# Optimization experiments

Hardware: AMD Instinct MI355X
Metric: run time of the kernel (lower is better)

## Reference

```python
import jax, jax.numpy as jnp
import numpy as np

B, NINP, NMAX, C = 32, 16, 128, 128

def conv1x1(x, w, b):
    # x: [B, cin, n, n], w: [cout, cin], b: [cout]
    return jnp.einsum('bchw,oc->bohw', x, w) + b[None, :, None, None]

def block(x, Msum, wa, ba, wb, bb, wc, bc):
    x1 = jax.nn.relu(conv1x1(x, wa, ba) * Msum)
    x2 = jax.nn.relu(conv1x1(x, wb, bb) * Msum)
    x1x2 = jnp.matmul(x1, x2) * Msum          # batched [B,C,n,n] @ [B,C,n,n]
    return jax.nn.relu(conv1x1(jnp.concatenate([x1x2, x], axis=1), wc, bc) * Msum)

def setup_inputs() -> dict:
    key = jax.random.key(0)
    ks = jax.random.split(key, 32)
    def w(k, o, i, s=0.05):
        return jax.random.normal(k, (o, i), dtype=jnp.float32) * s
    inp = {
        'X2': jax.random.normal(ks[0], (B, NINP, NMAX, NMAX), dtype=jnp.float32),
        'M':  jax.random.uniform(ks[1], (B, 2, NMAX, NMAX), dtype=jnp.float32),
        'w11': w(ks[2], C, NINP), 'b11': jnp.zeros((C,), jnp.float32),
        'w12': w(ks[3], C, NINP), 'b12': jnp.zeros((C,), jnp.float32),
        'w13': w(ks[4], C, C + NINP), 'b13': jnp.zeros((C,), jnp.float32),
        'w21': w(ks[5], C, C), 'b21': jnp.zeros((C,), jnp.float32),
        'w22': w(ks[6], C, C), 'b22': jnp.zeros((C,), jnp.float32),
        'w23': w(ks[7], C, 2 * C), 'b23': jnp.zeros((C,), jnp.float32),
        'w31': w(ks[8], C, C), 'b31': jnp.zeros((C,), jnp.float32),
        'w32': w(ks[9], C, C), 'b32': jnp.zeros((C,), jnp.float32),
        'w33': w(ks[10], C, 2 * C), 'b33': jnp.zeros((C,), jnp.float32),
        'h1w': w(ks[11], 32, 3 * C), 'h1b': jnp.zeros((32,), jnp.float32),
        'h2w': w(ks[12], 1, 32), 'h2b': jnp.zeros((1,), jnp.float32),
    }
    return inp

def reference(X2, M, w11, b11, w12, b12, w13, b13, w21, b21, w22, b22, w23, b23,
              w31, b31, w32, b32, w33, b33, h1w, h1b, h2w, h2b):
    Msum = jnp.sum(M, axis=1, keepdims=True)   # [B,1,n,n]
    Mdiag = M[:, 0:1]                          # [B,1,n,n]
    x = X2
    x = block(x, Msum, w11, b11, w12, b12, w13, b13)
    xo1 = jnp.sum(x * Mdiag, axis=(2, 3))      # [B,C]
    x = block(x, Msum, w21, b21, w22, b22, w23, b23)
    xo2 = jnp.sum(x * Mdiag, axis=(2, 3))
    x = block(x, Msum, w31, b31, w32, b32, w33, b33)
    xo3 = jnp.sum(x * Mdiag, axis=(2, 3))
    h = jnp.concatenate([xo1, xo2, xo3], axis=1)
    h = jax.nn.relu(h @ h1w.T + h1b)
    return h @ h2w.T + h2b                     # [B,1]
```

## Files before the change

### kernel.cpp

```cpp
#include <hip/hip_runtime.h>
#include <stdint.h>
#include <stddef.h>

#define NBATCH 32
#define HW     16384
#define CCH    128

typedef short bf16x8 __attribute__((ext_vector_type(8)));
typedef float f32x4  __attribute__((ext_vector_type(4)));

__device__ __forceinline__ float bf2f(unsigned short u){
    union { unsigned int i; float f; } v; v.i = ((unsigned int)u) << 16; return v.f;
}
__device__ __forceinline__ unsigned short f2bf(float f){
    union { float f; unsigned int i; } v; v.f = f;
    unsigned int x = v.i;
    x += 0x7fffu + ((x >> 16) & 1u);
    return (unsigned short)(x >> 16);
}

#define WPREP_TOTAL 319488
__global__ __launch_bounds__(256) void k_prep(
    const float* __restrict__ w11, const float* __restrict__ w12, const float* __restrict__ w13,
    const float* __restrict__ w21, const float* __restrict__ w22, const float* __restrict__ w23,
    const float* __restrict__ w31, const float* __restrict__ w32, const float* __restrict__ w33,
    unsigned short* __restrict__ wp)
{
    int i = blockIdx.x*256 + threadIdx.x;
    if(i >= WPREP_TOTAL) return;
    float v; int half;
    if(i < 16384){
        int j = i; half = (j >> 13) & 1;
        int r = (j >> 5) & 255, c = j & 31, col = c & 15;
        v = (r < 128) ? w11[r*16 + col] : w12[(r-128)*16 + col];
    } else if(i < 57344){
        int j = i - 16384; int ck = j >> 13; int jj = j & 8191;
        half = jj >> 12;
        int r = (jj >> 5) & 127, c = jj & 31;
        int col = (ck < 4) ? (ck*32 + c) : (128 + (c & 15));
        v = w13[r*144 + col];
    } else if(i < 122880){
        int j = i - 57344; int ck = j >> 14; int jj = j & 16383;
        half = jj >> 13;
        int r = (jj >> 5) & 255, c = jj & 31, col = ck*32 + c;
        v = (r < 128) ? w21[r*128 + col] : w22[(r-128)*128 + col];
    } else if(i < 188416){
        int j = i - 122880; int ck = j >> 13; int jj = j & 8191;
        half = jj >> 12;
        int r = (jj >> 5) & 127, c = jj & 31, col = ck*32 + c;
        v = w23[r*256 + col];
    } else if(i < 253952){
        int j = i - 188416; int ck = j >> 14; int jj = j & 16383;
        half = jj >> 13;
        int r = (jj >> 5) & 255, c = jj & 31, col = ck*32 + c;
        v = (r < 128) ? w31[r*128 + col] : w32[(r-128)*128 + col];
    } else {
        int j = i - 253952; int ck = j >> 13; int jj = j & 8191;
        half = jj >> 12;
        int r = (jj >> 5) & 127, c = jj & 31, col = ck*32 + c;
        v = w33[r*256 + col];
    }
    unsigned short hi = f2bf(v);
    wp[i] = half ? f2bf(v - bf2f(hi)) : hi;
}

__global__ __launch_bounds__(256) void k_xprep(const float* __restrict__ X2, unsigned short* __restrict__ X2b){
    int i = blockIdx.x*256 + threadIdx.x;
    int hw = i & (HW-1);
    int rest = i >> 14;
    int c = rest & 15, b = rest >> 4;
    float v = X2[i];
    unsigned short hi = f2bf(v);
    size_t dst = (size_t)b*32*HW + (size_t)c*HW + hw;
    X2b[dst] = hi;
    X2b[dst + (size_t)16*HW] = f2bf(v - bf2f(hi));
}

__global__ __launch_bounds__(256) void k_msum(const float* __restrict__ M, float* __restrict__ msum){
    int i = blockIdx.x*256 + threadIdx.x;
    int b = i >> 14, hw = i & (HW-1);
    msum[i] = M[(size_t)b*2*HW + hw] + M[(size_t)b*2*HW + HW + hw];
}

template<int NCH, int CIN, bool GX>
__global__ __launch_bounds__(256,2) void k_cab(
    const unsigned short* __restrict__ Wp,
    const unsigned short* __restrict__ xin,
    const float* __restrict__ ba, const float* __restrict__ bb,
    const float* __restrict__ msum,
    unsigned short* __restrict__ A, unsigned short* __restrict__ Bm, int b0)
{
    __shared__ unsigned short Wlh[256*40];
    __shared__ unsigned short Wll[256*40];
    __shared__ unsigned short Xt[128*40];
    const int bi = blockIdx.y, bg = b0 + bi;
    const int hw0 = blockIdx.x * 128;
    const int t = threadIdx.x;
    const int w = t >> 6, l = t & 63;
    const int lr = l & 15, lg = l >> 4;
    const unsigned short* xbase = xin + (size_t)(GX ? bg : bi)*CIN*HW;

    f32x4 acc[4][8];
    #pragma unroll
    for(int mf=0; mf<4; mf++)
        #pragma unroll
        for(int nf=0; nf<8; nf++) acc[mf][nf] = (f32x4){0.f,0.f,0.f,0.f};

    for(int ck=0; ck<NCH; ck++){
        if(ck) __syncthreads();
        #pragma unroll
        for(int it=0; it<8; it++){
            int idx = it*256 + t;
            int h = idx >> 10;
            int r = (idx >> 2) & 255, jg = (idx & 3) * 8;
            uint4 val = *reinterpret_cast<const uint4*>(Wp + (size_t)ck*16384 + h*8192 + r*32 + jg);
            unsigned short* dl = h ? Wll : Wlh;
            *reinterpret_cast<uint4*>(&dl[r*40 + jg]) = val;
        }
        #pragma unroll
        for(int it=0; it<2; it++){
            int hw = t & 127;
            int c0 = (it*2 + (t >> 7)) * 8;
            const unsigned short* xs = xbase + (size_t)(ck*32 + c0)*HW + hw0 + hw;
            unsigned short v[8];
            #pragma unroll
            for(int i=0;i<8;i++) v[i] = xs[(size_t)i*HW];
            uint4 pk;
            pk.x = (unsigned int)v[0] | ((unsigned int)v[1] << 16);
            pk.y = (unsigned int)v[2] | ((unsigned int)v[3] << 16);
            pk.z = (unsigned int)v[4] | ((unsigned int)v[5] << 16);
            pk.w = (unsigned int)v[6] | ((unsigned int)v[7] << 16);
            *reinterpret_cast<uint4*>(&Xt[hw*40 + c0]) = pk;
        }
        __syncthreads();
        bf16x8 ah[4], al[4];
        #pragma unroll
        for(int mf=0; mf<4; mf++){
            ah[mf] = *reinterpret_cast<const bf16x8*>(&Wlh[(w*64 + mf*16 + lr)*40 + lg*8]);
            al[mf] = *reinterpret_cast<const bf16x8*>(&Wll[(w*64 + mf*16 + lr)*40 + lg*8]);
        }
        #pragma unroll
        for(int nf=0; nf<8; nf++){
            bf16x8 bfr = *reinterpret_cast<const bf16x8*>(&Xt[(nf*16 + lr)*40 + lg*8]);
            #pragma unroll
            for(int mf=0; mf<4; mf++){
                acc[mf][nf] = __builtin_amdgcn_mfma_f32_16x16x32_bf16(ah[mf], bfr, acc[mf][nf], 0,0,0);
                acc[mf][nf] = __builtin_amdgcn_mfma_f32_16x16x32_bf16(al[mf], bfr, acc[mf][nf], 0,0,0);
            }
        }
    }
    float msv[8];
    #pragma unroll
    for(int nf=0; nf<8; nf++) msv[nf] = msum[(size_t)bg*HW + hw0 + nf*16 + lr];
    const float* bsel = (w < 2) ? ba : bb;
    unsigned short* dst = ((w < 2) ? A : Bm) + (size_t)bi*CCH*HW;
    const int rbase = (w & 1) * 64;
    #pragma unroll
    for(int mf=0; mf<4; mf++){
        #pragma unroll
        for(int reg=0; reg<4; reg++){
            int rl = rbase + mf*16 + lg*4 + reg;
            float bv = bsel[rl];
            #pragma unroll
            for(int nf=0; nf<8; nf++){
                float v2 = (acc[mf][nf][reg] + bv) * msv[nf];
                v2 = v2 > 0.f ? v2 : 0.f;
                dst[(size_t)rl*HW + hw0 + nf*16 + lr] = f2bf(v2);
            }
        }
    }
}

template<int NCHP, int NCHX, int CINX, bool GX>
__global__ __launch_bounds__(256,2) void k_cc(
    const unsigned short* __restrict__ Wp,
    const unsigned short* __restrict__ P,
    const unsigned short* __restrict__ x2,
    const float* __restrict__ bc,
    const float* __restrict__ msum, const float* __restrict__ M,
    unsigned short* __restrict__ Xout, float* __restrict__ xo,
    int b0, int xo_off)
{
    constexpr int NCH = NCHP + NCHX;
    __shared__ unsigned short Wlh[128*40];
    __shared__ unsigned short Wll[128*40];
    __shared__ unsigned short Xt[256*40];
    const int bi = blockIdx.y, bg = b0 + bi;
    const int hw0 = blockIdx.x * 256;
    const int t = threadIdx.x;
    const int w = t >> 6, l = t & 63;
    const int lr = l & 15, lg = l >> 4;
    const unsigned short* pbase = P  + (size_t)bi*CCH*HW;
    const unsigned short* xbase = x2 + (size_t)(GX ? bg : bi)*CINX*HW;

    f32x4 acc[8][4];
    #pragma unroll
    for(int mf=0; mf<8; mf++)
        #pragma unroll
        for(int nf=0; nf<4; nf++) acc[mf][nf] = (f32x4){0.f,0.f,0.f,0.f};

    for(int ck=0; ck<NCH; ck++){
        if(ck) __syncthreads();
        #pragma unroll
        for(int it=0; it<4; it++){
            int idx = it*256 + t;
            int h = idx >> 9;
            int r = (idx >> 2) & 127, jg = (idx & 3) * 8;
            uint4 val = *reinterpret_cast<const uint4*>(Wp + (size_t)ck*8192 + h*4096 + r*32 + jg);
            unsigned short* dl = h ? Wll : Wlh;
            *reinterpret_cast<uint4*>(&dl[r*40 + jg]) = val;
        }
        #pragma unroll
        for(int it=0; it<4; it++){
            int hw = t;
            int c0 = it * 8;
            const unsigned short* xs = (ck < NCHP)
                ? (pbase + (size_t)(ck*32 + c0)*HW + hw0 + hw)
                : (xbase + (size_t)((ck-NCHP)*32 + c0)*HW + hw0 + hw);
            unsigned short v[8];
            #pragma unroll
            for(int i=0;i<8;i++) v[i] = xs[(size_t)i*HW];
            uint4 pk;
            pk.x = (unsigned int)v[0] | ((unsigned int)v[1] << 16);
            pk.y = (unsigned int)v[2] | ((unsigned int)v[3] << 16);
            pk.z = (unsigned int)v[4] | ((unsigned int)v[5] << 16);
            pk.w = (unsigned int)v[6] | ((unsigned int)v[7] << 16);
            *reinterpret_cast<uint4*>(&Xt[hw*40 + c0]) = pk;
        }
        __syncthreads();
        bf16x8 bfr[4];
        #pragma unroll
        for(int nf=0; nf<4; nf++)
            bfr[nf] = *reinterpret_cast<const bf16x8*>(&Xt[(w*64 + nf*16 + lr)*40 + lg*8]);
        #pragma unroll
        for(int mf=0; mf<8; mf++){
            bf16x8 ah = *reinterpret_cast<const bf16x8*>(&Wlh[(mf*16 + lr)*40 + lg*8]);
            bf16x8 al = *reinterpret_cast<const bf16x8*>(&Wll[(mf*16 + lr)*40 + lg*8]);
            #pragma unroll
            for(int nf=0; nf<4; nf++){
                acc[mf][nf] = __builtin_amdgcn_mfma_f32_16x16x32_bf16(ah, bfr[nf], acc[mf][nf], 0,0,0);
                acc[mf][nf] = __builtin_amdgcn_mfma_f32_16x16x32_bf16(al, bfr[nf], acc[mf][nf], 0,0,0);
            }
        }
    }
    float msv[4], mdv[4];
    #pragma unroll
    for(int nf=0; nf<4; nf++){
        int hwi = hw0 + w*64 + nf*16 + lr;
        msv[nf] = msum[(size_t)bg*HW + hwi];
        mdv[nf] = M[(size_t)bg*2*HW + hwi];
    }
    unsigned short* dst = Xout + (size_t)bi*CCH*HW;
    #pragma unroll
    for(int mf=0; mf<8; mf++){
        float red[4] = {0.f,0.f,0.f,0.f};
        #pragma unroll
        for(int reg=0; reg<4; reg++){
            int row = mf*16 + lg*4 + reg;
            float bv = bc[row];
            #pragma unroll
            for(int nf=0; nf<4; nf++){
                float v2 = (acc[mf][nf][reg] + bv) * msv[nf];
                v2 = v2 > 0.f ? v2 : 0.f;
                dst[(size_t)row*HW + hw0 + w*64 + nf*16 + lr] = f2bf(v2);
                red[reg] += v2 * mdv[nf];
            }
        }
        #pragma unroll
        for(int reg=0; reg<4; reg++){
            float r = red[reg];
            r += __shfl_xor(r, 1);
            r += __shfl_xor(r, 2);
            r += __shfl_xor(r, 4);
            r += __shfl_xor(r, 8);
            if(lr == 0)
                atomicAdd(&xo[(size_t)bg*384 + xo_off + mf*16 + lg*4 + reg], r);
        }
    }
}

__global__ __launch_bounds__(256) void k_bmm(
    const unsigned short* __restrict__ A, const unsigned short* __restrict__ Bm,
    const float* __restrict__ msum, unsigned short* __restrict__ P, int b0)
{
    __shared__ unsigned short Bs[128*136];
    const int m  = blockIdx.x;
    const int bi = m >> 7;
    const int bg = b0 + bi;
    const unsigned short* Ab = A  + (size_t)m*HW;
    const unsigned short* Bb = Bm + (size_t)m*HW;
    unsigned short*       Pb = P  + (size_t)m*HW;
    const float* ms = msum + (size_t)bg*HW;
    const int t = threadIdx.x;

    #pragma unroll
    for(int it=0; it<8; it++){
        int task = it*256 + t;
        int j  = task & 127;
        int kg = task >> 7;
        unsigned short v[8];
        #pragma unroll
        for(int i=0;i<8;i++) v[i] = Bb[(size_t)(kg*8+i)*128 + j];
        uint4 pk;
        pk.x = (unsigned int)v[0] | ((unsigned int)v[1]<<16);
        pk.y = (unsigned int)v[2] | ((unsigned int)v[3]<<16);
        pk.z = (unsigned int)v[4] | ((unsigned int)v[5]<<16);
        pk.w = (unsigned int)v[6] | ((unsigned int)v[7]<<16);
        *reinterpret_cast<uint4*>(&Bs[j*136 + kg*8]) = pk;
    }
    __syncthreads();

    const int w  = t >> 6;
    const int l  = t & 63;
    const int lr = l & 15;
    const int lg = l >> 4;
    f32x4 acc[2][8];
    #pragma unroll
    for(int rt=0;rt<2;rt++)
        #pragma unroll
        for(int ct=0;ct<8;ct++) acc[rt][ct] = (f32x4){0.f,0.f,0.f,0.f};

    #pragma unroll 1
    for(int kk=0;kk<4;kk++){
        bf16x8 af[2];
        #pragma unroll
        for(int rt=0;rt<2;rt++){
            int row = w*32 + rt*16 + lr;
            af[rt] = *reinterpret_cast<const bf16x8*>(Ab + (size_t)row*128 + kk*32 + lg*8);
        }
        #pragma unroll
        for(int ct=0;ct<8;ct++){
            bf16x8 bfr = *reinterpret_cast<const bf16x8*>(&Bs[(ct*16+lr)*136 + kk*32 + lg*8]);
            acc[0][ct] = __builtin_amdgcn_mfma_f32_16x16x32_bf16(af[0], bfr, acc[0][ct], 0,0,0);
            acc[1][ct] = __builtin_amdgcn_mfma_f32_16x16x32_bf16(af[1], bfr, acc[1][ct], 0,0,0);
        }
    }
    #pragma unroll
    for(int rt=0;rt<2;rt++){
        #pragma unroll
        for(int ct=0;ct<8;ct++){
            #pragma unroll
            for(int r=0;r<4;r++){
                int row = w*32 + rt*16 + lg*4 + r;
                int col = ct*16 + lr;
                float v = acc[rt][ct][r] * ms[row*128 + col];
                Pb[(size_t)row*128 + col] = f2bf(v);
            }
        }
    }
}

__global__ __launch_bounds__(1024) void k_head(
    const float* __restrict__ xo, const float* __restrict__ h1w, const float* __restrict__ h1b,
    const float* __restrict__ h2w, const float* __restrict__ h2b, float* __restrict__ out)
{
    __shared__ float hbuf[NBATCH][32];
    const int t = threadIdx.x;
    const int b = t >> 5, j = t & 31;
    float a = h1b[j];
    #pragma unroll 8
    for(int k=0;k<384;k++) a += xo[b*384+k]*h1w[j*384+k];
    a = a > 0.f ? a : 0.f;
    hbuf[b][j] = a;
    __syncthreads();
    if(j == 0){
        float s = h2b[0];
        #pragma unroll
        for(int k=0;k<32;k++) s += hbuf[b][k]*h2w[k];
        out[b] = s;
    }
}

extern "C" void kernel_launch(void* const* d_in, const int* in_sizes, int n_in,
                              void* d_out, int out_size, void* d_ws, size_t ws_size,
                              hipStream_t stream)
{
    (void)in_sizes; (void)n_in; (void)out_size;
    const float* X2  = (const float*)d_in[0];
    const float* M   = (const float*)d_in[1];
    const float* w11 = (const float*)d_in[2];  const float* b11 = (const float*)d_in[3];
    const float* w12 = (const float*)d_in[4];  const float* b12 = (const float*)d_in[5];
    const float* w13 = (const float*)d_in[6];  const float* b13 = (const float*)d_in[7];
    const float* w21 = (const float*)d_in[8];  const float* b21 = (const float*)d_in[9];
    const float* w22 = (const float*)d_in[10]; const float* b22 = (const float*)d_in[11];
    const float* w23 = (const float*)d_in[12]; const float* b23 = (const float*)d_in[13];
    const float* w31 = (const float*)d_in[14]; const float* b31 = (const float*)d_in[15];
    const float* w32 = (const float*)d_in[16]; const float* b32 = (const float*)d_in[17];
    const float* w33 = (const float*)d_in[18]; const float* b33 = (const float*)d_in[19];
    const float* h1w = (const float*)d_in[20]; const float* h1b = (const float*)d_in[21];
    const float* h2w = (const float*)d_in[22]; const float* h2b = (const float*)d_in[23];
    float* out = (float*)d_out;

    char* ws = (char*)d_ws;
    size_t off = 0;
    float* msum = (float*)(ws + off); off += (size_t)NBATCH*HW*4;
    float* xo   = (float*)(ws + off); off += (size_t)NBATCH*384*4;
    unsigned short* wp  = (unsigned short*)(ws + off); off += (size_t)WPREP_TOTAL*2;
    off = (off + 255) & ~(size_t)255;
    unsigned short* X2b = (unsigned short*)(ws + off); off += (size_t)NBATCH*32*HW*2;
    off = (off + 255) & ~(size_t)255;

    int bc = 32;
    while (bc > 1 && off + 4ull*(size_t)bc*CCH*HW*2 > ws_size) bc >>= 1;
    size_t bufb = (size_t)bc*CCH*HW*2;
    unsigned short* bufA = (unsigned short*)(ws + off);
    unsigned short* bufB = (unsigned short*)(ws + off + bufb);
    unsigned short* bufP = (unsigned short*)(ws + off + 2*bufb);
    unsigned short* bufX = (unsigned short*)(ws + off + 3*bufb);

    const unsigned short* Wab1 = wp + 0;
    const unsigned short* Wc1  = wp + 16384;
    const unsigned short* Wab2 = wp + 57344;
    const unsigned short* Wc2  = wp + 122880;
    const unsigned short* Wab3 = wp + 188416;
    const unsigned short* Wc3  = wp + 253952;

    k_prep<<<(WPREP_TOTAL+255)/256, 256, 0, stream>>>(w11,w12,w13,w21,w22,w23,w31,w32,w33, wp);
    k_xprep<<<(NBATCH*16*HW)/256, 256, 0, stream>>>(X2, X2b);
    k_msum<<<(NBATCH*HW)/256, 256, 0, stream>>>(M, msum);
    hipMemsetAsync(xo, 0, (size_t)NBATCH*384*4, stream);

    for(int b0 = 0; b0 < NBATCH; b0 += bc){
        dim3 gab(HW/128, bc);
        dim3 gcc(HW/256, bc);
        dim3 gmat(bc*CCH);
        k_cab<1,32,true  ><<<gab, 256, 0, stream>>>(Wab1, X2b,  b11, b12, msum, bufA, bufB, b0);
        k_bmm<<<gmat, 256, 0, stream>>>(bufA, bufB, msum, bufP, b0);
        k_cc <4,1,32,true ><<<gcc, 256, 0, stream>>>(Wc1, bufP, X2b,  b13, msum, M, bufX, xo, b0, 0);
        k_cab<4,128,false><<<gab, 256, 0, stream>>>(Wab2, bufX, b21, b22, msum, bufA, bufB, b0);
        k_bmm<<<gmat, 256, 0, stream>>>(bufA, bufB, msum, bufP, b0);
        k_cc <4,4,128,false><<<gcc, 256, 0, stream>>>(Wc2, bufP, bufX, b23, msum, M, bufA, xo, b0, 128);
        k_cab<4,128,false><<<gab, 256, 0, stream>>>(Wab3, bufA, b31, b32, msum, bufB, bufP, b0);
        k_bmm<<<gmat, 256, 0, stream>>>(bufB, bufP, msum, bufX, b0);
        k_cc <4,4,128,false><<<gcc, 256, 0, stream>>>(Wc3, bufX, bufA, b33, msum, M, bufB, xo, b0, 256);
    }
    k_head<<<1, 1024, 0, stream>>>(xo, h1w, h1b, h2w, h2b, out);
}
```

Measured before the change: 1.413 ms.

## Register-prefetch next K-chunk in conv kernels and hoist A loads in bmm

The k_cab and k_cc 1x1-conv GEMMs now prefetch the next chunk's weights and activations into registers while the current chunk's MFMAs run, using a two-buffer register ping-pong. Activation loads are widened from scalar 16-bit reads to 4-wide uint2 reads and transposed into LDS in registers. Weight LDS tiles drop their padding (stride 32 instead of 40). In k_bmm, all A fragments are loaded from global before the B transpose and the k loop is fully unrolled. The changes aim to hide global-load latency and cut load instruction count, at the cost of more register pressure, which may reduce occupancy, and possible LDS bank conflicts from the unpadded weight layout.

```diff
diff --git a/kernel.cpp b/kernel.cpp
--- a/kernel.cpp
+++ b/kernel.cpp
@@ -17,6 +17,10 @@
     unsigned int x = v.i;
     x += 0x7fffu + ((x >> 16) & 1u);
     return (unsigned short)(x >> 16);
+}
+__device__ __forceinline__ unsigned int h16(uint2 u, int j){
+    unsigned int v = (j & 2) ? u.y : u.x;
+    return (j & 1) ? (v >> 16) : (v & 0xffffu);
 }
 
 #define WPREP_TOTAL 319488
@@ -90,14 +94,15 @@
     const float* __restrict__ msum,
     unsigned short* __restrict__ A, unsigned short* __restrict__ Bm, int b0)
 {
-    __shared__ unsigned short Wlh[256*40];
-    __shared__ unsigned short Wll[256*40];
+    __shared__ unsigned short Wl[16384];
     __shared__ unsigned short Xt[128*40];
     const int bi = blockIdx.y, bg = b0 + bi;
     const int hw0 = blockIdx.x * 128;
     const int t = threadIdx.x;
     const int w = t >> 6, l = t & 63;
     const int lr = l & 15, lg = l >> 4;
+    const int cg8 = t & 7;
+    const int h4  = t >> 3;
     const unsigned short* xbase = xin + (size_t)(GX ? bg : bi)*CIN*HW;
 
     f32x4 acc[4][8];
@@ -106,38 +111,38 @@
         #pragma unroll
         for(int nf=0; nf<8; nf++) acc[mf][nf] = (f32x4){0.f,0.f,0.f,0.f};
 
-    for(int ck=0; ck<NCH; ck++){
-        if(ck) __syncthreads();
-        #pragma unroll
-        for(int it=0; it<8; it++){
-            int idx = it*256 + t;
-            int h = idx >> 10;
-            int r = (idx >> 2) & 255, jg = (idx & 3) * 8;
-            uint4 val = *reinterpret_cast<const uint4*>(Wp + (size_t)ck*16384 + h*8192 + r*32 + jg);
-            unsigned short* dl = h ? Wll : Wlh;
-            *reinterpret_cast<uint4*>(&dl[r*40 + jg]) = val;
-        }
-        #pragma unroll
-        for(int it=0; it<2; it++){
-            int hw = t & 127;
-            int c0 = (it*2 + (t >> 7)) * 8;
-            const unsigned short* xs = xbase + (size_t)(ck*32 + c0)*HW + hw0 + hw;
-            unsigned short v[8];
-            #pragma unroll
-            for(int i=0;i<8;i++) v[i] = xs[(size_t)i*HW];
-            uint4 pk;
-            pk.x = (unsigned int)v[0] | ((unsigned int)v[1] << 16);
-            pk.y = (unsigned int)v[2] | ((unsigned int)v[3] << 16);
-            pk.z = (unsigned int)v[4] | ((unsigned int)v[5] << 16);
-            pk.w = (unsigned int)v[6] | ((unsigned int)v[7] << 16);
-            *reinterpret_cast<uint4*>(&Xt[hw*40 + c0]) = pk;
-        }
-        __syncthreads();
+    uint4 w0r[8], w1r[8];
+    uint2 x0r[4], x1r[4];
+
+    auto loadW = [&](int ck, uint4 (&wr)[8]){
+        const unsigned short* src = Wp + (size_t)ck*16384 + (size_t)t*8;
+        #pragma unroll
+        for(int r=0;r<8;r++) wr[r] = *reinterpret_cast<const uint4*>(src + (size_t)r*2048);
+    };
+    auto writeW = [&](uint4 (&wr)[8]){
+        #pragma unroll
+        for(int r=0;r<8;r++) *reinterpret_cast<uint4*>(&Wl[(r*256+t)*8]) = wr[r];
+    };
+    auto loadX = [&](int ck, uint2 (&xr)[4]){
+        const unsigned short* p = xbase + (size_t)(ck*32)*HW + hw0 + h4*4;
+        #pragma unroll
+        for(int i=0;i<4;i++) xr[i] = *reinterpret_cast<const uint2*>(p + (size_t)(cg8*4+i)*HW);
+    };
+    auto writeX = [&](uint2 (&xr)[4]){
+        #pragma unroll
+        for(int j=0;j<4;j++){
+            uint2 pk;
+            pk.x = h16(xr[0],j) | (h16(xr[1],j) << 16);
+            pk.y = h16(xr[2],j) | (h16(xr[3],j) << 16);
+            *reinterpret_cast<uint2*>(&Xt[(h4*4+j)*40 + cg8*4]) = pk;
+        }
+    };
+    auto compute = [&](){
         bf16x8 ah[4], al[4];
         #pragma unroll
         for(int mf=0; mf<4; mf++){
-            ah[mf] = *reinterpret_cast<const bf16x8*>(&Wlh[(w*64 + mf*16 + lr)*40 + lg*8]);
-            al[mf] = *reinterpret_cast<const bf16x8*>(&Wll[(w*64 + mf*16 + lr)*40 + lg*8]);
+            ah[mf] = *reinterpret_cast<const bf16x8*>(&Wl[(w*64 + mf*16 + lr)*32 + lg*8]);
+            al[mf] = *reinterpret_cast<const bf16x8*>(&Wl[8192 + (w*64 + mf*16 + lr)*32 + lg*8]);
         }
         #pragma unroll
         for(int nf=0; nf<8; nf++){
@@ -148,7 +153,21 @@
                 acc[mf][nf] = __builtin_amdgcn_mfma_f32_16x16x32_bf16(al[mf], bfr, acc[mf][nf], 0,0,0);
             }
         }
-    }
+    };
+    auto step = [&](int ck, uint4(&wc)[8], uint2(&xc)[4], uint4(&wn)[8], uint2(&xn)[4]){
+        writeW(wc); writeX(xc);
+        __syncthreads();
+        if(ck+1 < NCH){ loadW(ck+1, wn); loadX(ck+1, xn); }
+        compute();
+        __syncthreads();
+    };
+
+    loadW(0, w0r); loadX(0, x0r);
+    for(int ck=0; ck<NCH; ck+=2){
+        step(ck, w0r, x0r, w1r, x1r);
+        if(ck+1 < NCH) step(ck+1, w1r, x1r, w0r, x0r);
+    }
+
     float msv[8];
     #pragma unroll
     for(int nf=0; nf<8; nf++) msv[nf] = msum[(size_t)bg*HW + hw0 + nf*16 + lr];
@@ -182,14 +201,15 @@
     int b0, int xo_off)
 {
     constexpr int NCH = NCHP + NCHX;
-    __shared__ unsigned short Wlh[128*40];
-    __shared__ unsigned short Wll[128*40];
+    __shared__ unsigned short Wl[8192];
     __shared__ unsigned short Xt[256*40];
     const int bi = blockIdx.y, bg = b0 + bi;
     const int hw0 = blockIdx.x * 256;
     const int t = threadIdx.x;
     const int w = t >> 6, l = t & 63;
     const int lr = l & 15, lg = l >> 4;
+    const int cg = t & 3;
+    const int h4 = t >> 2;
     const unsigned short* pbase = P  + (size_t)bi*CCH*HW;
     const unsigned short* xbase = x2 + (size_t)(GX ? bg : bi)*CINX*HW;
 
@@ -199,50 +219,67 @@
         #pragma unroll
         for(int nf=0; nf<4; nf++) acc[mf][nf] = (f32x4){0.f,0.f,0.f,0.f};
 
-    for(int ck=0; ck<NCH; ck++){
-        if(ck) __syncthreads();
-        #pragma unroll
-        for(int it=0; it<4; it++){
-            int idx = it*256 + t;
-            int h = idx >> 9;
-            int r = (idx >> 2) & 127, jg = (idx & 3) * 8;
-            uint4 val = *reinterpret_cast<const uint4*>(Wp + (size_t)ck*8192 + h*4096 + r*32 + jg);
-            unsigned short* dl = h ? Wll : Wlh;
-            *reinterpret_cast<uint4*>(&dl[r*40 + jg]) = val;
-        }
-        #pragma unroll
-        for(int it=0; it<4; it++){
-            int hw = t;
-            int c0 = it * 8;
-            const unsigned short* xs = (ck < NCHP)
-                ? (pbase + (size_t)(ck*32 + c0)*HW + hw0 + hw)
-                : (xbase + (size_t)((ck-NCHP)*32 + c0)*HW + hw0 + hw);
-            unsigned short v[8];
-            #pragma unroll
-            for(int i=0;i<8;i++) v[i] = xs[(size_t)i*HW];
+    uint4 w0r[4], w1r[4];
+    uint2 x0r[8], x1r[8];
+
+    auto loadW = [&](int ck, uint4 (&wr)[4]){
+        const unsigned short* src = Wp + (size_t)ck*8192 + (size_t)t*8;
+        #pragma unroll
+        for(int r=0;r<4;r++) wr[r] = *reinterpret_cast<const uint4*>(src + (size_t)r*2048);
+    };
+    auto writeW = [&](uint4 (&wr)[4]){
+        #pragma unroll
+        for(int r=0;r<4;r++) *reinterpret_cast<uint4*>(&Wl[(r*256+t)*8]) = wr[r];
+    };
+    auto loadX = [&](int ck, uint2 (&xr)[8]){
+        const unsigned short* xs = (ck < NCHP)
+            ? (pbase + (size_t)(ck*32)*HW)
+            : (xbase + (size_t)((ck-NCHP)*32)*HW);
+        const unsigned short* p = xs + hw0 + h4*4;
+        #pragma unroll
+        for(int i=0;i<8;i++) xr[i] = *reinterpret_cast<const uint2*>(p + (size_t)(cg*8+i)*HW);
+    };
+    auto writeX = [&](uint2 (&xr)[8]){
+        #pragma unroll
+        for(int j=0;j<4;j++){
             uint4 pk;
-            pk.x = (unsigned int)v[0] | ((unsigned int)v[1] << 16);
-            pk.y = (unsigned int)v[2] | ((unsigned int)v[3] << 16);
-            pk.z = (unsigned int)v[4] | ((unsigned int)v[5] << 16);
-            pk.w = (unsigned int)v[6] | ((unsigned int)v[7] << 16);
-            *reinterpret_cast<uint4*>(&Xt[hw*40 + c0]) = pk;
-        }
-        __syncthreads();
+            pk.x = h16(xr[0],j) | (h16(xr[1],j) << 16);
+            pk.y = h16(xr[2],j) | (h16(xr[3],j) << 16);
+            pk.z = h16(xr[4],j) | (h16(xr[5],j) << 16);
+            pk.w = h16(xr[6],j) | (h16(xr[7],j) << 16);
+            *reinterpret_cast<uint4*>(&Xt[(h4*4+j)*40 + cg*8]) = pk;
+        }
+    };
+    auto compute = [&](){
         bf16x8 bfr[4];
         #pragma unroll
         for(int nf=0; nf<4; nf++)
             bfr[nf] = *reinterpret_cast<const bf16x8*>(&Xt[(w*64 + nf*16 + lr)*40 + lg*8]);
         #pragma unroll
         for(int mf=0; mf<8; mf++){
-            bf16x8 ah = *reinterpret_cast<const bf16x8*>(&Wlh[(mf*16 + lr)*40 + lg*8]);
-            bf16x8 al = *reinterpret_cast<const bf16x8*>(&Wll[(mf*16 + lr)*40 + lg*8]);
+            bf16x8 ah = *reinterpret_cast<const bf16x8*>(&Wl[(mf*16 + lr)*32 + lg*8]);
+            bf16x8 al = *reinterpret_cast<const bf16x8*>(&Wl[4096 + (mf*16 + lr)*32 + lg*8]);
             #pragma unroll
             for(int nf=0; nf<4; nf++){
                 acc[mf][nf] = __builtin_amdgcn_mfma_f32_16x16x32_bf16(ah, bfr[nf], acc[mf][nf], 0,0,0);
                 acc[mf][nf] = __builtin_amdgcn_mfma_f32_16x16x32_bf16(al, bfr[nf], acc[mf][nf], 0,0,0);
             }
         }
-    }
+    };
+    auto step = [&](int ck, uint4(&wc)[4], uint2(&xc)[8], uint4(&wn)[4], uint2(&xn)[8]){
+        writeW(wc); writeX(xc);
+        __syncthreads();
+        if(ck+1 < NCH){ loadW(ck+1, wn); loadX(ck+1, xn); }
+        compute();
+        __syncthreads();
+    };
+
+    loadW(0, w0r); loadX(0, x0r);
+    for(int ck=0; ck<NCH; ck+=2){
+        step(ck, w0r, x0r, w1r, x1r);
+        if(ck+1 < NCH) step(ck+1, w1r, x1r, w0r, x0r);
+    }
+
     float msv[4], mdv[4];
     #pragma unroll
     for(int nf=0; nf<4; nf++){
@@ -292,6 +329,17 @@
     unsigned short*       Pb = P  + (size_t)m*HW;
     const float* ms = msum + (size_t)bg*HW;
     const int t = threadIdx.x;
+    const int w  = t >> 6;
+    const int l  = t & 63;
+    const int lr = l & 15;
+    const int lg = l >> 4;
+
+    bf16x8 af[4][2];
+    #pragma unroll
+    for(int kk=0;kk<4;kk++)
+        #pragma unroll
+        for(int rt=0;rt<2;rt++)
+            af[kk][rt] = *reinterpret_cast<const bf16x8*>(Ab + (size_t)(w*32 + rt*16 + lr)*128 + kk*32 + lg*8);
 
     #pragma unroll
     for(int it=0; it<8; it++){
@@ -310,29 +358,19 @@
     }
     __syncthreads();
 
-    const int w  = t >> 6;
-    const int l  = t & 63;
-    const int lr = l & 15;
-    const int lg = l >> 4;
     f32x4 acc[2][8];
     #pragma unroll
     for(int rt=0;rt<2;rt++)
         #pragma unroll
         for(int ct=0;ct<8;ct++) acc[rt][ct] = (f32x4){0.f,0.f,0.f,0.f};
 
-    #pragma unroll 1
+    #pragma unroll
     for(int kk=0;kk<4;kk++){
-        bf16x8 af[2];
-        #pragma unroll
-        for(int rt=0;rt<2;rt++){
-            int row = w*32 + rt*16 + lr;
-            af[rt] = *reinterpret_cast<const bf16x8*>(Ab + (size_t)row*128 + kk*32 + lg*8);
-        }
         #pragma unroll
         for(int ct=0;ct<8;ct++){
             bf16x8 bfr = *reinterpret_cast<const bf16x8*>(&Bs[(ct*16+lr)*136 + kk*32 + lg*8]);
-            acc[0][ct] = __builtin_amdgcn_mfma_f32_16x16x32_bf16(af[0], bfr, acc[0][ct], 0,0,0);
-            acc[1][ct] = __builtin_amdgcn_mfma_f32_16x16x32_bf16(af[1], bfr, acc[1][ct], 0,0,0);
+            acc[0][ct] = __builtin_amdgcn_mfma_f32_16x16x32_bf16(af[kk][0], bfr, acc[0][ct], 0,0,0);
+            acc[1][ct] = __builtin_amdgcn_mfma_f32_16x16x32_bf16(af[kk][1], bfr, acc[1][ct], 0,0,0);
         }
     }
     #pragma unroll
```

Result: slower. 2.054 ms (+45.4%).
